# Optimization experiments

Hardware: AMD Instinct MI355X
Metric: run time of the kernel (lower is better)

The kernel has to match this reference:

```python
import jax, jax.numpy as jnp
import numpy as np
import math

NUM_FREQS = 16  # module init num_freqs


def posenc(x, nf):
    # x [..., D] -> [..., D*2*nf]
    freqs = 2.0 ** jnp.arange(nf, dtype=x.dtype)
    xf = x[..., None] * freqs  # [..., D, nf]
    enc = jnp.concatenate([jnp.sin(xf), jnp.cos(xf)], axis=-1)  # [..., D, 2nf]
    return enc.reshape(x.shape[:-1] + (x.shape[-1] * 2 * nf,))


def plucker(rays):
    # rays [..., 6] = [origin, direction] -> [d_norm, cross(o, d_norm)]
    o, dv = rays[..., :3], rays[..., 3:]
    dn = dv / (jnp.linalg.norm(dv, axis=-1, keepdims=True) + 1e-8)
    return jnp.concatenate([dn, jnp.cross(o, dn)], axis=-1)


def grid_sample_bilinear(img, grid):
    # img [N,C,H,W], grid [N,Hg,Wg,2] in [-1,1], align_corners=True, zeros padding
    N, C, H, W = img.shape
    x = (grid[..., 0] + 1.0) * 0.5 * (W - 1)
    y = (grid[..., 1] + 1.0) * 0.5 * (H - 1)
    x0 = jnp.floor(x); x1 = x0 + 1.0
    y0 = jnp.floor(y); y1 = y0 + 1.0
    wx1 = x - x0; wx0 = 1.0 - wx1
    wy1 = y - y0; wy0 = 1.0 - wy1

    def gather(ix, iy):
        valid = ((ix >= 0) & (ix <= W - 1) & (iy >= 0) & (iy <= H - 1)).astype(img.dtype)
        ixc = jnp.clip(ix, 0, W - 1).astype(jnp.int32)
        iyc = jnp.clip(iy, 0, H - 1).astype(jnp.int32)
        vals = jax.vmap(lambda im, iyn, ixn: im[:, iyn, ixn])(img, iyc, ixc)  # [N,C,Hg,Wg]
        return vals * valid[:, None]

    return (gather(x0, y0) * (wx0 * wy0)[:, None]
            + gather(x1, y0) * (wx1 * wy0)[:, None]
            + gather(x0, y1) * (wx0 * wy1)[:, None]
            + gather(x1, y1) * (wx1 * wy1)[:, None])


def _forward(xref, mask_ref, ray_points, rays, R, T, focal, W1, b1, W2, b2, Wv, bv, Wd):
    F = NUM_FREQS
    b, n, hw, c = xref.shape
    d = ray_points.shape[3]
    res = int(math.sqrt(hw))
    # mask (already at res x res; nearest resize is identity)
    xref = xref * mask_ref.reshape(b, n, hw, 1)
    # project sample points into all n+1 camera NDC frames
    pts = ray_points[:, 0]  # [b,hw,d,3]
    p_view = jnp.einsum('bhdk,bvkj->bvhdj', pts, R) + T[:, :, None, None]  # [b,n+1,hw,d,3]
    ndc = focal[:, :, None, None, None] * p_view[..., :2] / p_view[..., 2:3]
    grid = jax.lax.stop_gradient(jnp.clip(jnp.nan_to_num(-ndc[:, 1:]), -1.2, 1.2))
    grid = grid.reshape(b * n, hw, d, 2)
    img = xref.reshape(b * n, res, res, c).transpose(0, 3, 1, 2)  # [(bn),c,res,res]
    pf = grid_sample_bilinear(img, grid)  # [(bn),c,hw,d]
    plane_features = pf.reshape(b, n, c, hw, d).transpose(0, 1, 3, 4, 2)  # [b,n,hw,d,c]

    xyz_iv = p_view                       # view-space points [b,n+1,hw,d,3]
    xyz_iv_enc = posenc(xyz_iv, F)        # [b,n+1,hw,d,6F]

    # target rays (view 0) expressed in every view frame
    o_t, d_t = rays[:, 0, :, :3], rays[:, 0, :, 3:]
    o_iv = jnp.einsum('bhk,bvkj->bvhj', o_t, R) + T[:, :, None]
    d_iv = jnp.einsum('bhk,bvkj->bvhj', d_t, R)
    cam_iv = jnp.concatenate([o_iv, d_iv], -1)[:, 1:]  # [b,n,hw,6]
    cam_iv = jnp.broadcast_to(cam_iv[:, :, :, None, :], (b, n, hw, d, 6))
    cam_iv_enc = posenc(plucker(cam_iv), F // 2)  # [b,n,hw,d,6F]

    xyz_grid = jnp.broadcast_to(xyz_iv_enc[:, :1], (b, n, hw, d, xyz_iv_enc.shape[-1]))
    # reference-view ray origins in target frame
    o_r = rays[:, 1:, :, :3]
    o_tg = jnp.einsum('bnhk,bkj->bnhj', o_r, R[:, 0]) + T[:, 0][:, None, None]
    cam_feat = jnp.broadcast_to(o_tg[:, :, :, None, :], (b, n, hw, d, 3))
    cam_feat_enc = posenc(cam_feat, F)

    plane_in = jnp.concatenate([plane_features, xyz_iv_enc[:, 1:], xyz_iv[:, 1:],
                                cam_iv_enc, cam_iv[..., 3:]], axis=-1)  # [b,n,hw,d,326]
    h = jax.nn.silu(plane_in @ W1 + b1)
    pf_final = h @ W2 + b2  # [b,n,hw,d,C]

    attn_in = jnp.concatenate([plane_features, xyz_grid,
                               jnp.broadcast_to(xyz_iv[:, :1], (b, n, hw, d, 3)),
                               cam_feat, cam_feat_enc], axis=-1)  # [b,n,hw,d,326]
    attn = jax.nn.softmax(attn_in @ Wv + bv, axis=1)  # softmax over views
    fused = (pf_final * attn).sum(1)  # [b,hw,d,C]
    out = fused @ Wd  # decoder (no bias) -> [b,hw,d,1]
    return jnp.concatenate([fused, out], axis=-1), attn


def setup_inputs() -> dict:
    B, N, RES, D, C = 1, 4, 32, 32, 128
    HW = RES * RES
    IN_DIM = C + NUM_FREQS * 3 * 4 + 6  # 326
    key = jax.random.key(0)
    ks = jax.random.split(key, 16)
    xref = jax.random.normal(ks[0], (B, N, HW, C), jnp.float32)
    mask_ref = (jax.random.uniform(ks[1], (B, N, RES, RES)) > 0.1).astype(jnp.float32)
    ray_points = jax.random.uniform(ks[2], (B, 1, HW, D, 3), minval=-0.5, maxval=0.5)
    o = jax.random.uniform(ks[3], (B, N + 1, HW, 3), minval=-0.2, maxval=0.2)
    dirs = jax.random.normal(ks[4], (B, N + 1, HW, 3))
    dirs = dirs / jnp.linalg.norm(dirs, axis=-1, keepdims=True)
    rays = jnp.concatenate([o, dirs], -1)
    R = jnp.linalg.qr(jax.random.normal(ks[5], (B, N + 1, 3, 3)))[0]
    T = jnp.concatenate([jax.random.uniform(ks[6], (B, N + 1, 2), minval=-0.2, maxval=0.2),
                         jax.random.uniform(ks[7], (B, N + 1, 1), minval=2.0, maxval=2.5)], -1)
    focal = jax.random.uniform(ks[8], (B, N + 1), minval=0.8, maxval=1.2)
    W1 = jax.random.normal(ks[9], (IN_DIM, C)) / np.sqrt(IN_DIM)
    b1 = jnp.zeros((C,), jnp.float32)
    W2 = jax.random.normal(ks[10], (C, C)) / np.sqrt(C)
    b2 = jnp.zeros((C,), jnp.float32)
    Wv = jax.random.normal(ks[11], (IN_DIM, 1)) / np.sqrt(IN_DIM)
    bv = jnp.zeros((1,), jnp.float32)
    Wd = jax.random.normal(ks[12], (C, 1)) * 0.01  # zero_module in source; small random for meaningful baseline
    return {"xref": xref, "mask_ref": mask_ref, "ray_points": ray_points, "rays": rays,
            "R": R, "T": T, "focal": focal, "W1": W1, "b1": b1, "W2": W2, "b2": b2,
            "Wv": Wv, "bv": bv, "Wd": Wd}


def reference(xref, mask_ref, ray_points, rays, R, T, focal, W1, b1, W2, b2, Wv, bv, Wd):
    return _forward(xref, mask_ref, ray_points, rays, R, T, focal, W1, b1, W2, b2, Wv, bv, Wd)
```

## Files before the change

### kernel.cpp

```cpp
#include <hip/hip_runtime.h>
#include <hip/hip_bf16.h>
#include <math.h>

#define XH 1024
#define XD 32
#define XC 128
#define XK 326

typedef __attribute__((ext_vector_type(8))) short bf16x8;
typedef __attribute__((ext_vector_type(4))) float f32x4;

__device__ __forceinline__ unsigned short f2b(float f) {
  unsigned u = __float_as_uint(f);
  return (unsigned short)((u + 0x7FFFu + ((u >> 16) & 1u)) >> 16);
}
__device__ __forceinline__ float b2f(unsigned short b) {
  return __uint_as_float(((unsigned)b) << 16);
}
__device__ __forceinline__ unsigned pk2bf(float v0, float v1) {
  __hip_bfloat162 h = __float22bfloat162_rn(make_float2(v0, v1));
  return *reinterpret_cast<unsigned*>(&h);
}

#define WT1 (12 * 8 * 64)
#define WT2 (4 * 8 * 64)

__global__ void prep_frags(const float* __restrict__ W1,
                           const float* __restrict__ W2,
                           unsigned int* __restrict__ ws) {
  int f = blockIdx.x * 256 + threadIdx.x;
  if (f >= WT1 + WT2) return;
  const float* W; int KMAX; int fl; size_t hoff, loff;
  if (f < WT1) { W = W1; KMAX = XK; fl = f; hoff = 0; loff = WT1; }
  else { W = W2; KMAX = XC; fl = f - WT1; hoff = 2 * (size_t)WT1; loff = 2 * (size_t)WT1 + WT2; }
  int l = fl & 63, ct = (fl >> 6) & 7, kc = fl >> 9;
  int c = ct * 16 + (l & 15);
  int kbase = kc * 32 + 8 * (l >> 4);
  unsigned hi[4], lo[4];
  #pragma unroll
  for (int jj = 0; jj < 4; ++jj) {
    int k0 = kbase + 2 * jj;
    float w0 = (k0     < KMAX) ? W[k0 * XC + c]       : 0.f;
    float w1 = (k0 + 1 < KMAX) ? W[(k0 + 1) * XC + c] : 0.f;
    unsigned short h0 = f2b(w0); unsigned short l0 = f2b(w0 - b2f(h0));
    unsigned short h1 = f2b(w1); unsigned short l1 = f2b(w1 - b2f(h1));
    hi[jj] = (unsigned)h0 | ((unsigned)h1 << 16);
    lo[jj] = (unsigned)l0 | ((unsigned)l1 << 16);
  }
  uint4 vh; vh.x = hi[0]; vh.y = hi[1]; vh.z = hi[2]; vh.w = hi[3];
  uint4 vl; vl.x = lo[0]; vl.y = lo[1]; vl.z = lo[2]; vl.w = lo[3];
  *(uint4*)(ws + (hoff + fl) * 4) = vh;
  *(uint4*)(ws + (loff + fl) * 4) = vl;
}


__global__ __launch_bounds__(512, 4)
void nerf_main(const float* __restrict__ xref,
               const float* __restrict__ mask,
               const float* __restrict__ rpts,
               const float* __restrict__ rays,
               const float* __restrict__ Rm,
               const float* __restrict__ Tm,
               const float* __restrict__ focp,
               const float* __restrict__ b1p,
               const float* __restrict__ b2p,
               const float* __restrict__ Wvp,
               const float* __restrict__ bvp,
               const float* __restrict__ Wdp,
               const bf16x8* __restrict__ wfrag,
               float* __restrict__ out0,
               float* __restrict__ out1)
{
  const int h = blockIdx.x;
  const int tid = threadIdx.x;

  __shared__ float sR[5][3][3];
  __shared__ float sT[5][3];
  __shared__ float sFoc[5];
  __shared__ float sRay[5][6];
  __shared__ float sOiv[5][3];
  __shared__ float sDiv[5][3];
  __shared__ float sPlk[4][6];
  __shared__ float sOtg[4][3];
  __shared__ float sPv[5][32][3];
  __shared__ float sBc[4][32][4];
  __shared__ int   sBp[4][32][4];
  __shared__ float sWv[XK];
  __shared__ float sAt[32];
  __shared__ float sBt[4];
  __shared__ float sLogit[4][32];
  __shared__ float sAw[4][32];
  __shared__ float sOutPart[4][32];
  __shared__ __align__(16) unsigned short sEnc2[4][128];
  __shared__ __align__(16) unsigned char uMem[32896];
  unsigned short* sFcHi = (unsigned short*)uMem;
  unsigned short* sFcLo = (unsigned short*)(uMem + 16512);
  unsigned short* sHbHi = (unsigned short*)(uMem + 16512);
  unsigned short* sHbLo = sHbHi + 32 * 128;
  float*          sOut  = (float*)uMem;

  for (int i = tid; i < 45; i += 512) ((float*)sR)[i] = Rm[i];
  for (int i = tid; i < 15; i += 512) ((float*)sT)[i] = Tm[i];
  for (int i = tid; i < 5;  i += 512) sFoc[i] = focp[i];
  for (int i = tid; i < 30; i += 512) { int v = i / 6, j = i % 6; sRay[v][j] = rays[(v*XH + h)*6 + j]; }
  for (int i = tid; i < XK; i += 512) sWv[i] = Wvp[i];
  __syncthreads();

  if (tid < 160) {
    int v = tid >> 5, d = tid & 31;
    float p0 = rpts[(h*XD + d)*3 + 0];
    float p1 = rpts[(h*XD + d)*3 + 1];
    float p2 = rpts[(h*XD + d)*3 + 2];
    #pragma unroll
    for (int j = 0; j < 3; ++j)
      sPv[v][d][j] = p0*sR[v][0][j] + p1*sR[v][1][j] + p2*sR[v][2][j] + sT[v][j];
  } else if (tid < 165) {
    int v = tid - 160;
    #pragma unroll
    for (int j = 0; j < 3; ++j) {
      sOiv[v][j] = sRay[0][0]*sR[v][0][j] + sRay[0][1]*sR[v][1][j] + sRay[0][2]*sR[v][2][j] + sT[v][j];
      sDiv[v][j] = sRay[0][3]*sR[v][0][j] + sRay[0][4]*sR[v][1][j] + sRay[0][5]*sR[v][2][j];
    }
  }
  __syncthreads();

  if (tid < 4) {
    int n = tid;
    float d0 = sDiv[n+1][0], d1 = sDiv[n+1][1], d2 = sDiv[n+1][2];
    float inv = 1.f / (sqrtf(d0*d0 + d1*d1 + d2*d2) + 1e-8f);
    float n0 = d0*inv, n1 = d1*inv, n2 = d2*inv;
    float o0 = sOiv[n+1][0], o1 = sOiv[n+1][1], o2 = sOiv[n+1][2];
    sPlk[n][0] = n0; sPlk[n][1] = n1; sPlk[n][2] = n2;
    sPlk[n][3] = o1*n2 - o2*n1;
    sPlk[n][4] = o2*n0 - o0*n2;
    sPlk[n][5] = o0*n1 - o1*n0;
    #pragma unroll
    for (int j = 0; j < 3; ++j)
      sOtg[n][j] = sRay[1+n][0]*sR[0][0][j] + sRay[1+n][1]*sR[0][1][j] + sRay[1+n][2]*sR[0][2][j] + sT[0][j];
  }
  if (tid >= 32 && tid < 160) {
    int idx = tid - 32, n = idx >> 5, d = idx & 31, v = n + 1;
    float px = sPv[v][d][0], py = sPv[v][d][1], pz = sPv[v][d][2], fo = sFoc[v];
    float gx = -(fo*px)/pz, gy = -(fo*py)/pz;
    if (isnan(gx)) gx = 0.f;
    if (isnan(gy)) gy = 0.f;
    gx = fminf(fmaxf(gx, -1.2f), 1.2f);
    gy = fminf(fmaxf(gy, -1.2f), 1.2f);
    float x = (gx + 1.f)*15.5f, y = (gy + 1.f)*15.5f;
    float x0f = floorf(x), y0f = floorf(y);
    float wx1 = x - x0f, wx0 = 1.f - wx1;
    float wy1 = y - y0f, wy0 = 1.f - wy1;
    int x0i = (int)x0f, y0i = (int)y0f;
    bool vx0 = (x0f >=  0.f) & (x0f <= 31.f);
    bool vx1 = (x0f >= -1.f) & (x0f <= 30.f);
    bool vy0 = (y0f >=  0.f) & (y0f <= 31.f);
    bool vy1 = (y0f >= -1.f) & (y0f <= 30.f);
    int x0c = min(max(x0i, 0), 31), x1c = min(max(x0i + 1, 0), 31);
    int y0c = min(max(y0i, 0), 31), y1c = min(max(y0i + 1, 0), 31);
    int p00 = y0c*32 + x0c, p10 = y0c*32 + x1c, p01 = y1c*32 + x0c, p11 = y1c*32 + x1c;
    sBc[n][d][0] = wx0*wy0*((vx0 && vy0) ? mask[n*XH + p00] : 0.f);
    sBc[n][d][1] = wx1*wy0*((vx1 && vy0) ? mask[n*XH + p10] : 0.f);
    sBc[n][d][2] = wx0*wy1*((vx0 && vy1) ? mask[n*XH + p01] : 0.f);
    sBc[n][d][3] = wx1*wy1*((vx1 && vy1) ? mask[n*XH + p11] : 0.f);
    sBp[n][d][0] = p00; sBp[n][d][1] = p10; sBp[n][d][2] = p01; sBp[n][d][3] = p11;
  }
  if (tid >= 256) {
    int t = tid - 256;
    int d = t >> 3, sub = t & 7;
    float p = 0.f;
    for (int kk = sub * 12; kk < sub * 12 + 12; ++kk) {
      int comp = kk >> 5, idx = kk & 31;
      float ang = sPv[0][d][comp] * (float)(1 << (idx & 15));
      float ev = (idx < 16) ? __sinf(ang) : __cosf(ang);
      p += ev * sWv[128 + kk];
    }
    if (sub == 0)
      for (int j = 0; j < 3; ++j) p += sPv[0][d][j] * sWv[224 + j];
    #pragma unroll
    for (int o = 1; o < 8; o <<= 1) p += __shfl_xor(p, o);
    if (sub == 0) sAt[d] = p;
  }
  __syncthreads();

  {
    int n = tid >> 7, off = tid & 127;
    float val = 0.f;
    if (off >= 3 && off < 99) {
      int kk = off - 3;
      int comp = kk >> 4, idx = kk & 15;
      float ang = sPlk[n][comp] * (float)(1 << (idx & 7));
      val = (idx < 8) ? __sinf(ang) : __cosf(ang);
    } else if (off >= 99 && off < 102) {
      val = sDiv[n + 1][off - 99];
    }
    sEnc2[n][off] = f2b(val);
  }
  if (tid >= 256 && tid < 288) {
    int t = tid - 256, n = t >> 3, sub = t & 7;
    float p = 0.f;
    for (int kk = sub * 12; kk < sub * 12 + 12; ++kk) {
      int comp = kk >> 5, idx = kk & 31;
      float ang = sOtg[n][comp] * (float)(1 << (idx & 15));
      float ev = (idx < 16) ? __sinf(ang) : __cosf(ang);
      p += ev * sWv[230 + kk];
    }
    if (sub == 0) {
      for (int j = 0; j < 3; ++j) p += sOtg[n][j] * sWv[227 + j];
      p += bvp[0];
    }
    #pragma unroll
    for (int o = 1; o < 8; o <<= 1) p += __shfl_xor(p, o);
    if (sub == 0) sBt[n] = p;
  }
  __syncthreads();

  const int w = tid >> 6, lane = tid & 63;
  const int rt = w & 3, cg = w >> 2;
  const int lrow = lane & 15, lg = lane >> 4;
  float bias1[4];
  #pragma unroll
  for (int ct = 0; ct < 4; ++ct) bias1[ct] = b1p[cg * 64 + ct * 16 + lrow];

  f32x4 acc1[2][4];
  #pragma unroll
  for (int rf = 0; rf < 2; ++rf)
    #pragma unroll
    for (int ct = 0; ct < 4; ++ct) acc1[rf][ct] = (f32x4){0.f, 0.f, 0.f, 0.f};

  const int brow = tid >> 2;
  const int bn = brow & 3, bd = brow >> 2;
  const int kloc0 = (tid & 3) * 16;
  float plog = 0.f;

  #pragma unroll 1
  for (int chunk = 0; chunk < 2; ++chunk) {
    int kg0 = chunk * 64 + kloc0;
    {
      float v[16];
      const float* bc = sBc[bn][bd];
      const int*   bp = sBp[bn][bd];
      const float* xb = xref + bn * XH * XC;
      #pragma unroll
      for (int q = 0; q < 4; ++q) {
        float4 a0 = *(const float4*)(xb + bp[0] * XC + kg0 + 4 * q);
        float4 a1 = *(const float4*)(xb + bp[1] * XC + kg0 + 4 * q);
        float4 a2 = *(const float4*)(xb + bp[2] * XC + kg0 + 4 * q);
        float4 a3 = *(const float4*)(xb + bp[3] * XC + kg0 + 4 * q);
        #pragma unroll
        for (int j = 0; j < 4; ++j)
          v[4 * q + j] = bc[0]*(&a0.x)[j] + bc[1]*(&a1.x)[j]
                       + bc[2]*(&a2.x)[j] + bc[3]*(&a3.x)[j];
      }
      #pragma unroll
      for (int j = 0; j < 16; ++j) plog += v[j] * sWv[kg0 + j];
      #pragma unroll
      for (int q = 0; q < 2; ++q) {
        unsigned ph[4], pl[4];
        #pragma unroll
        for (int j = 0; j < 4; ++j) {
          float v0 = v[8 * q + 2 * j], v1 = v[8 * q + 2 * j + 1];
          unsigned hp = pk2bf(v0, v1);
          float r0 = v0 - b2f((unsigned short)(hp & 0xFFFF));
          float r1 = v1 - b2f((unsigned short)(hp >> 16));
          ph[j] = hp;
          pl[j] = pk2bf(r0, r1);
        }
        int gidx = (brow * 64 + kloc0 + 8 * q) ^ ((brow & 7) << 3);
        *(uint4*)&sFcHi[gidx] = *(uint4*)ph;
        *(uint4*)&sFcLo[gidx] = *(uint4*)pl;
      }
    }
    if (chunk == 1) {
      float p = plog;
      p += __shfl_xor(p, 1);
      p += __shfl_xor(p, 2);
      if ((tid & 3) == 0) sLogit[bn][bd] = p;
    }
    __syncthreads();

    #pragma unroll
    for (int sk = 0; sk < 2; ++sk) {
      const int kc = chunk * 2 + sk;
      const int r0 = rt * 32 + lrow;
      const int ai0 = (r0 * 64 + sk * 32 + 8 * lg) ^ ((r0 & 7) << 3);
      const int ai1 = ai0 + 16 * 64;
      bf16x8 ah0 = *(const bf16x8*)&sFcHi[ai0];
      bf16x8 ah1 = *(const bf16x8*)&sFcHi[ai1];
      bf16x8 al0 = *(const bf16x8*)&sFcLo[ai0];
      bf16x8 al1 = *(const bf16x8*)&sFcLo[ai1];
      #pragma unroll
      for (int ct = 0; ct < 4; ++ct) {
        int bidx = (kc * 8 + cg * 4 + ct) * 64 + lane;
        bf16x8 bh = wfrag[bidx];
        bf16x8 bl = wfrag[WT1 + bidx];
        acc1[0][ct] = __builtin_amdgcn_mfma_f32_16x16x32_bf16(ah0, bh, acc1[0][ct], 0, 0, 0);
        acc1[0][ct] = __builtin_amdgcn_mfma_f32_16x16x32_bf16(ah0, bl, acc1[0][ct], 0, 0, 0);
        acc1[0][ct] = __builtin_amdgcn_mfma_f32_16x16x32_bf16(al0, bh, acc1[0][ct], 0, 0, 0);
        acc1[1][ct] = __builtin_amdgcn_mfma_f32_16x16x32_bf16(ah1, bh, acc1[1][ct], 0, 0, 0);
        acc1[1][ct] = __builtin_amdgcn_mfma_f32_16x16x32_bf16(ah1, bl, acc1[1][ct], 0, 0, 0);
        acc1[1][ct] = __builtin_amdgcn_mfma_f32_16x16x32_bf16(al1, bh, acc1[1][ct], 0, 0, 0);
      }
    }
    __syncthreads();
  }

  if (tid < 32) {
    int d = tid;
    float l0 = sLogit[0][d] + sAt[d] + sBt[0];
    float l1 = sLogit[1][d] + sAt[d] + sBt[1];
    float l2 = sLogit[2][d] + sAt[d] + sBt[2];
    float l3 = sLogit[3][d] + sAt[d] + sBt[3];
    float m = fmaxf(fmaxf(l0, l1), fmaxf(l2, l3));
    float e0 = __expf(l0 - m), e1 = __expf(l1 - m), e2 = __expf(l2 - m), e3 = __expf(l3 - m);
    float inv = 1.f / (e0 + e1 + e2 + e3);
    float w0 = e0*inv, w1 = e1*inv, w2 = e2*inv, w3 = e3*inv;
    sAw[0][d] = w0; sAw[1][d] = w1; sAw[2][d] = w2; sAw[3][d] = w3;
    out1[(0*XH + h)*XD + d] = w0;
    out1[(1*XH + h)*XD + d] = w1;
    out1[(2*XH + h)*XD + d] = w2;
    out1[(3*XH + h)*XD + d] = w3;
  }

  {
    const int r0c = rt * 32 + lrow;
    const int nn = r0c & 3;
    const int dd = r0c >> 2;
    const float* pv0 = sPv[nn + 1][dd];
    const float* pv1 = sPv[nn + 1][dd + 4];
    const unsigned short* enc = sEnc2[nn];
    const float m0 = (lg & 1) ? 256.f : 1.f;
    const bool usn = (lg < 2);

    auto mfma4 = [&](int kc, bf16x8 A0, bf16x8 A1) {
      #pragma unroll
      for (int ct = 0; ct < 4; ++ct) {
        int bidx = (kc * 8 + cg * 4 + ct) * 64 + lane;
        bf16x8 bh = wfrag[bidx];
        bf16x8 bl = wfrag[WT1 + bidx];
        acc1[0][ct] = __builtin_amdgcn_mfma_f32_16x16x32_bf16(A0, bh, acc1[0][ct], 0, 0, 0);
        acc1[0][ct] = __builtin_amdgcn_mfma_f32_16x16x32_bf16(A0, bl, acc1[0][ct], 0, 0, 0);
        acc1[1][ct] = __builtin_amdgcn_mfma_f32_16x16x32_bf16(A1, bh, acc1[1][ct], 0, 0, 0);
        acc1[1][ct] = __builtin_amdgcn_mfma_f32_16x16x32_bf16(A1, bl, acc1[1][ct], 0, 0, 0);
      }
    };
    auto trigf = [&](const float* pv, int comp) -> bf16x8 {
      float pA = pv[comp] * m0;
      unsigned ph[4];
      #pragma unroll
      for (int mj = 0; mj < 4; ++mj) {
        float a0f = pA * (float)(1 << (2 * mj));
        float a1f = pA * (float)(1 << (2 * mj + 1));
        float v0 = usn ? __sinf(a0f) : __cosf(a0f);
        float v1 = usn ? __sinf(a1f) : __cosf(a1f);
        ph[mj] = pk2bf(v0, v1);
      }
      union { unsigned u[4]; bf16x8 f; } cv;
      cv.u[0] = ph[0]; cv.u[1] = ph[1]; cv.u[2] = ph[2]; cv.u[3] = ph[3];
      return cv.f;
    };
    auto encf = [&](int off) -> bf16x8 {
      return *(const bf16x8*)&enc[off + lg * 8];
    };

    mfma4(4, trigf(pv0, 0), trigf(pv1, 0));
    mfma4(5, trigf(pv0, 1), trigf(pv1, 1));
    mfma4(6, trigf(pv0, 2), trigf(pv1, 2));
    {
      bf16x8 e0 = encf(0);
      bf16x8 e1 = e0;
      if (lg == 0) {
        e0[0] = (short)f2b(pv0[0]); e0[1] = (short)f2b(pv0[1]); e0[2] = (short)f2b(pv0[2]);
        e1[0] = (short)f2b(pv1[0]); e1[1] = (short)f2b(pv1[1]); e1[2] = (short)f2b(pv1[2]);
      }
      mfma4(7, e0, e1);
    }
    { bf16x8 e = encf(32); mfma4(8, e, e); }
    { bf16x8 e = encf(64); mfma4(9, e, e); }
    { bf16x8 e = encf(96); mfma4(10, e, e); }
  }
  __syncthreads();

  #pragma unroll
  for (int rf = 0; rf < 2; ++rf) {
    int d = (rt * 2 + rf) * 4 + lg;
    float a0 = sAw[0][d], a1 = sAw[1][d], a2 = sAw[2][d], a3 = sAw[3][d];
    #pragma unroll
    for (int ct = 0; ct < 4; ++ct) {
      int c = cg * 64 + ct * 16 + lrow;
      float x0 = acc1[rf][ct][0] + bias1[ct];
      float x1 = acc1[rf][ct][1] + bias1[ct];
      float x2 = acc1[rf][ct][2] + bias1[ct];
      float x3 = acc1[rf][ct][3] + bias1[ct];
      float hb = a0 * __fdividef(x0, 1.f + __expf(-x0))
               + a1 * __fdividef(x1, 1.f + __expf(-x1))
               + a2 * __fdividef(x2, 1.f + __expf(-x2))
               + a3 * __fdividef(x3, 1.f + __expf(-x3));
      unsigned short hh = f2b(hb);
      unsigned short hl = f2b(hb - b2f(hh));
      int idx = (d * 128 + c) ^ ((d & 7) << 3);
      sHbHi[idx] = hh; sHbLo[idx] = hl;
    }
  }
  __syncthreads();

  const int rt2 = w & 1, cg2 = w >> 1;
  float bias2[2], wdv[2];
  #pragma unroll
  for (int cti = 0; cti < 2; ++cti) {
    int c = cg2 * 32 + cti * 16 + lrow;
    bias2[cti] = b2p[c]; wdv[cti] = Wdp[c];
  }
  f32x4 acc2[2];
  acc2[0] = (f32x4){0.f, 0.f, 0.f, 0.f};
  acc2[1] = (f32x4){0.f, 0.f, 0.f, 0.f};
  {
    const int ar = rt2 * 16 + lrow;
    #pragma unroll
    for (int kc = 0; kc < 4; ++kc) {
      int aidx = (ar * 128 + kc * 32 + 8 * lg) ^ ((ar & 7) << 3);
      bf16x8 ah = *(const bf16x8*)&sHbHi[aidx];
      bf16x8 al = *(const bf16x8*)&sHbLo[aidx];
      #pragma unroll
      for (int cti = 0; cti < 2; ++cti) {
        int bidx = (kc * 8 + cg2 * 2 + cti) * 64 + lane;
        bf16x8 bh = wfrag[2 * WT1 + bidx];
        bf16x8 bl = wfrag[2 * WT1 + WT2 + bidx];
        acc2[cti] = __builtin_amdgcn_mfma_f32_16x16x32_bf16(ah, bh, acc2[cti], 0, 0, 0);
        acc2[cti] = __builtin_amdgcn_mfma_f32_16x16x32_bf16(ah, bl, acc2[cti], 0, 0, 0);
        acc2[cti] = __builtin_amdgcn_mfma_f32_16x16x32_bf16(al, bh, acc2[cti], 0, 0, 0);
      }
    }
  }

  {
    float part[4] = {0.f, 0.f, 0.f, 0.f};
    #pragma unroll
    for (int cti = 0; cti < 2; ++cti) {
      int c = cg2 * 32 + cti * 16 + lrow;
      #pragma unroll
      for (int i = 0; i < 4; ++i) {
        int d = rt2 * 16 + lg * 4 + i;
        float fv = acc2[cti][i] + bias2[cti];
        sOut[d * 129 + c] = fv;
        part[i] += fv * wdv[cti];
      }
    }
    #pragma unroll
    for (int i = 0; i < 4; ++i) {
      float p = part[i];
      #pragma unroll
      for (int o = 1; o < 16; o <<= 1) p += __shfl_xor(p, o);
      if (lrow == 0) sOutPart[cg2][rt2 * 16 + lg * 4 + i] = p;
    }
  }
  __syncthreads();
  if (tid < 32)
    sOut[tid * 129 + 128] =
      sOutPart[0][tid] + sOutPart[1][tid] + sOutPart[2][tid] + sOutPart[3][tid];
  __syncthreads();
  {
    const float4* src = (const float4*)sOut;
    float4* dst = (float4*)(out0 + (size_t)h * (XD * 129));
    for (int i = tid; i < (XD * 129) / 4; i += 512) dst[i] = src[i];
  }
}

extern "C" void kernel_launch(void* const* d_in, const int* in_sizes, int n_in,
                              void* d_out, int out_size, void* d_ws, size_t ws_size,
                              hipStream_t stream) {
  const float* xref = (const float*)d_in[0];
  const float* mask = (const float*)d_in[1];
  const float* rpts = (const float*)d_in[2];
  const float* rays = (const float*)d_in[3];
  const float* Rm   = (const float*)d_in[4];
  const float* Tm   = (const float*)d_in[5];
  const float* foc  = (const float*)d_in[6];
  const float* W1   = (const float*)d_in[7];
  const float* b1   = (const float*)d_in[8];
  const float* W2   = (const float*)d_in[9];
  const float* b2   = (const float*)d_in[10];
  const float* Wv   = (const float*)d_in[11];
  const float* bv   = (const float*)d_in[12];
  const float* Wd   = (const float*)d_in[13];
  float* out0 = (float*)d_out;
  float* out1 = out0 + (size_t)XH * XD * 129;

  hipLaunchKernelGGL(prep_frags, dim3(32), dim3(256), 0, stream,
                     W1, W2, (unsigned int*)d_ws);
  hipLaunchKernelGGL(nerf_main, dim3(XH), dim3(512), 0, stream,
                     xref, mask, rpts, rays, Rm, Tm, foc,
                     b1, b2, Wv, bv, Wd, (const bf16x8*)d_ws, out0, out1);
}
```

Baseline: 74.19 us.

## Gather full feature tile into LDS once, then run first-layer MFMA without mid-loop barriers

The bilinear gather of reference features now fills the whole 128-wide K dimension into shared memory in one pass, replacing two chunks of 64 with a barrier between gather and MFMA in each. The shared buffer grows from about 32 KB to 64 KB. The first-layer MFMA loop then runs over four K slices after a single barrier, and weight-fragment addressing is rewritten to use base pointers with constant offsets. This removes two synchronisations and lets all gather loads be issued together, at the cost of doubled LDS use, which may reduce how many blocks fit per CU.

```diff
diff --git a/kernel.cpp b/kernel.cpp
--- a/kernel.cpp
+++ b/kernel.cpp
@@ -92,10 +92,10 @@
   __shared__ float sAw[4][32];
   __shared__ float sOutPart[4][32];
   __shared__ __align__(16) unsigned short sEnc2[4][128];
-  __shared__ __align__(16) unsigned char uMem[32896];
+  __shared__ __align__(16) unsigned char uMem[65536];
   unsigned short* sFcHi = (unsigned short*)uMem;
-  unsigned short* sFcLo = (unsigned short*)(uMem + 16512);
-  unsigned short* sHbHi = (unsigned short*)(uMem + 16512);
+  unsigned short* sFcLo = (unsigned short*)(uMem + 32768);
+  unsigned short* sHbHi = (unsigned short*)(uMem + 32768);
   unsigned short* sHbLo = sHbHi + 32 * 128;
   float*          sOut  = (float*)uMem;
 
@@ -214,95 +214,57 @@
   }
   __syncthreads();
 
-  const int w = tid >> 6, lane = tid & 63;
-  const int rt = w & 3, cg = w >> 2;
-  const int lrow = lane & 15, lg = lane >> 4;
-  float bias1[4];
-  #pragma unroll
-  for (int ct = 0; ct < 4; ++ct) bias1[ct] = b1p[cg * 64 + ct * 16 + lrow];
-
-  f32x4 acc1[2][4];
-  #pragma unroll
-  for (int rf = 0; rf < 2; ++rf)
-    #pragma unroll
-    for (int ct = 0; ct < 4; ++ct) acc1[rf][ct] = (f32x4){0.f, 0.f, 0.f, 0.f};
-
   const int brow = tid >> 2;
   const int bn = brow & 3, bd = brow >> 2;
   const int kloc0 = (tid & 3) * 16;
   float plog = 0.f;
 
-  #pragma unroll 1
-  for (int chunk = 0; chunk < 2; ++chunk) {
-    int kg0 = chunk * 64 + kloc0;
-    {
-      float v[16];
-      const float* bc = sBc[bn][bd];
-      const int*   bp = sBp[bn][bd];
-      const float* xb = xref + bn * XH * XC;
+  {
+    const float* bc = sBc[bn][bd];
+    const int*   bp = sBp[bn][bd];
+    const float* xb = xref + bn * XH * XC;
+    #pragma unroll
+    for (int chunk = 0; chunk < 2; ++chunk) {
+      int kg = chunk * 64 + kloc0;
+      float vv[16];
       #pragma unroll
       for (int q = 0; q < 4; ++q) {
-        float4 a0 = *(const float4*)(xb + bp[0] * XC + kg0 + 4 * q);
-        float4 a1 = *(const float4*)(xb + bp[1] * XC + kg0 + 4 * q);
-        float4 a2 = *(const float4*)(xb + bp[2] * XC + kg0 + 4 * q);
-        float4 a3 = *(const float4*)(xb + bp[3] * XC + kg0 + 4 * q);
+        float4 a0 = *(const float4*)(xb + bp[0] * XC + kg + 4 * q);
+        float4 a1 = *(const float4*)(xb + bp[1] * XC + kg + 4 * q);
+        float4 a2 = *(const float4*)(xb + bp[2] * XC + kg + 4 * q);
+        float4 a3 = *(const float4*)(xb + bp[3] * XC + kg + 4 * q);
         #pragma unroll
         for (int j = 0; j < 4; ++j)
-          v[4 * q + j] = bc[0]*(&a0.x)[j] + bc[1]*(&a1.x)[j]
-                       + bc[2]*(&a2.x)[j] + bc[3]*(&a3.x)[j];
-      }
-      #pragma unroll
-      for (int j = 0; j < 16; ++j) plog += v[j] * sWv[kg0 + j];
+          vv[4 * q + j] = bc[0]*(&a0.x)[j] + bc[1]*(&a1.x)[j]
+                        + bc[2]*(&a2.x)[j] + bc[3]*(&a3.x)[j];
+      }
+      #pragma unroll
+      for (int j = 0; j < 16; ++j) plog += vv[j] * sWv[kg + j];
       #pragma unroll
       for (int q = 0; q < 2; ++q) {
         unsigned ph[4], pl[4];
         #pragma unroll
         for (int j = 0; j < 4; ++j) {
-          float v0 = v[8 * q + 2 * j], v1 = v[8 * q + 2 * j + 1];
+          float v0 = vv[8 * q + 2 * j], v1 = vv[8 * q + 2 * j + 1];
           unsigned hp = pk2bf(v0, v1);
           float r0 = v0 - b2f((unsigned short)(hp & 0xFFFF));
           float r1 = v1 - b2f((unsigned short)(hp >> 16));
           ph[j] = hp;
           pl[j] = pk2bf(r0, r1);
         }
-        int gidx = (brow * 64 + kloc0 + 8 * q) ^ ((brow & 7) << 3);
+        int gidx = (brow * 128 + kg + 8 * q) ^ ((brow & 7) << 3);
         *(uint4*)&sFcHi[gidx] = *(uint4*)ph;
         *(uint4*)&sFcLo[gidx] = *(uint4*)pl;
       }
     }
-    if (chunk == 1) {
+    {
       float p = plog;
       p += __shfl_xor(p, 1);
       p += __shfl_xor(p, 2);
       if ((tid & 3) == 0) sLogit[bn][bd] = p;
     }
-    __syncthreads();
-
-    #pragma unroll
-    for (int sk = 0; sk < 2; ++sk) {
-      const int kc = chunk * 2 + sk;
-      const int r0 = rt * 32 + lrow;
-      const int ai0 = (r0 * 64 + sk * 32 + 8 * lg) ^ ((r0 & 7) << 3);
-      const int ai1 = ai0 + 16 * 64;
-      bf16x8 ah0 = *(const bf16x8*)&sFcHi[ai0];
-      bf16x8 ah1 = *(const bf16x8*)&sFcHi[ai1];
-      bf16x8 al0 = *(const bf16x8*)&sFcLo[ai0];
-      bf16x8 al1 = *(const bf16x8*)&sFcLo[ai1];
-      #pragma unroll
-      for (int ct = 0; ct < 4; ++ct) {
-        int bidx = (kc * 8 + cg * 4 + ct) * 64 + lane;
-        bf16x8 bh = wfrag[bidx];
-        bf16x8 bl = wfrag[WT1 + bidx];
-        acc1[0][ct] = __builtin_amdgcn_mfma_f32_16x16x32_bf16(ah0, bh, acc1[0][ct], 0, 0, 0);
-        acc1[0][ct] = __builtin_amdgcn_mfma_f32_16x16x32_bf16(ah0, bl, acc1[0][ct], 0, 0, 0);
-        acc1[0][ct] = __builtin_amdgcn_mfma_f32_16x16x32_bf16(al0, bh, acc1[0][ct], 0, 0, 0);
-        acc1[1][ct] = __builtin_amdgcn_mfma_f32_16x16x32_bf16(ah1, bh, acc1[1][ct], 0, 0, 0);
-        acc1[1][ct] = __builtin_amdgcn_mfma_f32_16x16x32_bf16(ah1, bl, acc1[1][ct], 0, 0, 0);
-        acc1[1][ct] = __builtin_amdgcn_mfma_f32_16x16x32_bf16(al1, bh, acc1[1][ct], 0, 0, 0);
-      }
-    }
-    __syncthreads();
-  }
+  }
+  __syncthreads();
 
   if (tid < 32) {
     int d = tid;
@@ -321,6 +283,43 @@
     out1[(3*XH + h)*XD + d] = w3;
   }
 
+  const int w = tid >> 6, lane = tid & 63;
+  const int rt = w & 3, cg = w >> 2;
+  const int lrow = lane & 15, lg = lane >> 4;
+  float bias1[4];
+  #pragma unroll
+  for (int ct = 0; ct < 4; ++ct) bias1[ct] = b1p[cg * 64 + ct * 16 + lrow];
+
+  f32x4 acc1[2][4];
+  #pragma unroll
+  for (int rf = 0; rf < 2; ++rf)
+    #pragma unroll
+    for (int ct = 0; ct < 4; ++ct) acc1[rf][ct] = (f32x4){0.f, 0.f, 0.f, 0.f};
+
+  #pragma unroll
+  for (int sk = 0; sk < 4; ++sk) {
+    const int r0 = rt * 32 + lrow;
+    const int ai0 = (r0 * 128 + sk * 32 + 8 * lg) ^ ((r0 & 7) << 3);
+    const int ai1 = ai0 + 16 * 128;
+    bf16x8 ah0 = *(const bf16x8*)&sFcHi[ai0];
+    bf16x8 ah1 = *(const bf16x8*)&sFcHi[ai1];
+    bf16x8 al0 = *(const bf16x8*)&sFcLo[ai0];
+    bf16x8 al1 = *(const bf16x8*)&sFcLo[ai1];
+    const bf16x8* wkh = wfrag + (sk * 8 + cg * 4) * 64 + lane;
+    const bf16x8* wkl = wkh + WT1;
+    #pragma unroll
+    for (int ct = 0; ct < 4; ++ct) {
+      bf16x8 bh = wkh[ct * 64];
+      bf16x8 bl = wkl[ct * 64];
+      acc1[0][ct] = __builtin_amdgcn_mfma_f32_16x16x32_bf16(ah0, bh, acc1[0][ct], 0, 0, 0);
+      acc1[0][ct] = __builtin_amdgcn_mfma_f32_16x16x32_bf16(ah0, bl, acc1[0][ct], 0, 0, 0);
+      acc1[0][ct] = __builtin_amdgcn_mfma_f32_16x16x32_bf16(al0, bh, acc1[0][ct], 0, 0, 0);
+      acc1[1][ct] = __builtin_amdgcn_mfma_f32_16x16x32_bf16(ah1, bh, acc1[1][ct], 0, 0, 0);
+      acc1[1][ct] = __builtin_amdgcn_mfma_f32_16x16x32_bf16(ah1, bl, acc1[1][ct], 0, 0, 0);
+      acc1[1][ct] = __builtin_amdgcn_mfma_f32_16x16x32_bf16(al1, bh, acc1[1][ct], 0, 0, 0);
+    }
+  }
+
   {
     const int r0c = rt * 32 + lrow;
     const int nn = r0c & 3;
@@ -332,11 +331,12 @@
     const bool usn = (lg < 2);
 
     auto mfma4 = [&](int kc, bf16x8 A0, bf16x8 A1) {
+      const bf16x8* wkh = wfrag + (kc * 8 + cg * 4) * 64 + lane;
+      const bf16x8* wkl = wkh + WT1;
       #pragma unroll
       for (int ct = 0; ct < 4; ++ct) {
-        int bidx = (kc * 8 + cg * 4 + ct) * 64 + lane;
-        bf16x8 bh = wfrag[bidx];
-        bf16x8 bl = wfrag[WT1 + bidx];
+        bf16x8 bh = wkh[ct * 64];
+        bf16x8 bl = wkl[ct * 64];
         acc1[0][ct] = __builtin_amdgcn_mfma_f32_16x16x32_bf16(A0, bh, acc1[0][ct], 0, 0, 0);
         acc1[0][ct] = __builtin_amdgcn_mfma_f32_16x16x32_bf16(A0, bl, acc1[0][ct], 0, 0, 0);
         acc1[1][ct] = __builtin_amdgcn_mfma_f32_16x16x32_bf16(A1, bh, acc1[1][ct], 0, 0, 0);
@@ -420,11 +420,12 @@
       int aidx = (ar * 128 + kc * 32 + 8 * lg) ^ ((ar & 7) << 3);
       bf16x8 ah = *(const bf16x8*)&sHbHi[aidx];
       bf16x8 al = *(const bf16x8*)&sHbLo[aidx];
+      const bf16x8* wkh = wfrag + 2 * WT1 + (kc * 8 + cg2 * 2) * 64 + lane;
+      const bf16x8* wkl = wkh + WT2;
       #pragma unroll
       for (int cti = 0; cti < 2; ++cti) {
-        int bidx = (kc * 8 + cg2 * 2 + cti) * 64 + lane;
-        bf16x8 bh = wfrag[2 * WT1 + bidx];
-        bf16x8 bl = wfrag[2 * WT1 + WT2 + bidx];
+        bf16x8 bh = wkh[cti * 64];
+        bf16x8 bl = wkl[cti * 64];
         acc2[cti] = __builtin_amdgcn_mfma_f32_16x16x32_bf16(ah, bh, acc2[cti], 0, 0, 0);
         acc2[cti] = __builtin_amdgcn_mfma_f32_16x16x32_bf16(ah, bl, acc2[cti], 0, 0, 0);
         acc2[cti] = __builtin_amdgcn_mfma_f32_16x16x32_bf16(al, bh, acc2[cti], 0, 0, 0);
```

Result: faster. 71.63 us (-3.4%).
